# Optimization experiments

Measured on AMD Instinct MI355X. Metric: run time of the kernel, lower is better.

The kernel has to match this reference:

```python
import jax, jax.numpy as jnp
import numpy as np

K_WIN = 3  # fixed kernel width in the original module
PAD = (K_WIN - 1) // 2


def setup_inputs() -> dict:
    key = jax.random.key(0)
    k1, k2, k3 = jax.random.split(key, 3)
    B, L, D, T = 32, 2048, 256, 64
    x = jax.random.normal(k1, (B, L, D), dtype=jnp.float32)
    C = jax.random.normal(k2, (T, D), dtype=jnp.float32) * (1.0 / np.sqrt(D))
    W_den = jax.random.normal(k3, (D, K_WIN * D), dtype=jnp.float32) * (1.0 / np.sqrt(D))
    b_den = jnp.zeros((K_WIN * D,), dtype=jnp.float32)
    return {"x": x, "C": C, "W_den": W_den, "b_den": b_den}


def reference(x, C, W_den, b_den):
    B, L, D = x.shape
    T = C.shape[0]
    # kc = relu(C @ W + b): [T, k*D] -> [T, k, D]
    kc = jax.nn.relu(C @ W_den + b_den).reshape(T, K_WIN, D)
    # att = x @ C^T: [B, L, T]
    att = jnp.einsum('bld,td->blt', x, C)
    # per-position dynamic kernels: [B, L, k, D]
    ki = jnp.einsum('blt,tkd->blkd', att, kc)
    # sliding windows of padded x: [B, L, k, D]
    x_pad = jnp.pad(x, ((0, 0), (PAD, PAD), (0, 0)))
    windows = jnp.stack([x_pad[:, j:j + L, :] for j in range(K_WIN)], axis=2)
    # windowed multiply-sum over k: [B, L, D]
    return jnp.sum(windows * ki, axis=2)
```

## Files before the change

kernel.cpp:

```cpp
#include <hip/hip_runtime.h>

#define B_  32
#define L_  2048
#define D_  256
#define T_  64
#define KW  3
#define ROWS  16
#define XROWS 18

typedef float f32x4 __attribute__((ext_vector_type(4)));
typedef short s16x8 __attribute__((ext_vector_type(8)));
typedef short s16x4 __attribute__((ext_vector_type(4)));

__device__ __forceinline__ short f2bf(float f) {
    unsigned u = __builtin_bit_cast(unsigned, f);
    u += 0x7FFFu + ((u >> 16) & 1u);
    return (short)(u >> 16);
}
__device__ __forceinline__ float bf2f(short s) {
    unsigned u = ((unsigned)(unsigned short)s) << 16;
    return __builtin_bit_cast(float, u);
}

__global__ __launch_bounds__(256) void prep_kernel(const float* __restrict__ C,
                                                   const float* __restrict__ W,
                                                   const float* __restrict__ bias,
                                                   short* __restrict__ CbfPk,
                                                   short* __restrict__ kcPk) {
    __shared__ float Ws[256 * 16];
    const int tid = threadIdx.x;

    if (blockIdx.x < 16) {
        const int i0 = (blockIdx.x * 256 + tid) * 4;
        const int t = i0 >> 8, d = i0 & 255;
        const f32x4 v = *(const f32x4*)(C + i0);
        s16x4 s;
        s[0] = f2bf(v[0]); s[1] = f2bf(v[1]); s[2] = f2bf(v[2]); s[3] = f2bf(v[3]);
        const int tt = t >> 4, c = t & 15, ks = d >> 5, gg = (d >> 3) & 3, e = d & 7;
        *(s16x4*)&CbfPk[(((tt * 8 + ks) * 4 + gg) * 16 + c) * 8 + e] = s;
        return;
    }

    const int nb = blockIdx.x - 16;
    const int n0 = nb * 16;

    for (int idx = tid; idx < 256 * 16; idx += 256) {
        const int dd = idx >> 4, nl = idx & 15;
        Ws[idx] = W[dd * (KW * D_) + n0 + nl];
    }
    __syncthreads();

    const int t  = tid >> 2;
    const int nl = tid & 3;
    float acc[4];
    #pragma unroll
    for (int i = 0; i < 4; ++i) acc[i] = bias[n0 + nl + 4 * i];

    const float* Crow = C + t * D_;
    for (int dd = 0; dd < D_; ++dd) {
        const float cv = Crow[dd];
        #pragma unroll
        for (int i = 0; i < 4; ++i)
            acc[i] = fmaf(cv, Ws[dd * 16 + nl + 4 * i], acc[i]);
    }
    const int ks = t >> 5, gg = (t >> 3) & 3, e = t & 7;
    #pragma unroll
    for (int i = 0; i < 4; ++i) {
        const int cc = nl + 4 * i;
        kcPk[(((nb * 2 + ks) * 4 + gg) * 16 + cc) * 8 + e] = f2bf(fmaxf(acc[i], 0.f));
    }
}

#define XST 264
#define ATS 72

__global__ __launch_bounds__(256, 8) void main_kernel(const float* __restrict__ x,
                                                      const short* __restrict__ CbfPk,
                                                      const short* __restrict__ kcPk,
                                                      float* __restrict__ out) {
    __shared__ short xs[XROWS * XST];
    __shared__ short atts[ROWS * ATS];

    const int tid  = threadIdx.x;
    const int w    = tid >> 6;
    const int lane = tid & 63;
    const int c    = lane & 15;
    const int g    = lane >> 4;
    const int l0   = blockIdx.x * ROWS;
    const int b    = blockIdx.y;

    const f32x4* x4 = (const f32x4*)(x + (size_t)b * L_ * D_);
    for (int idx = tid; idx < XROWS * 64; idx += 256) {
        const int row = idx >> 6;
        const int d4  = idx & 63;
        const int l   = l0 - 1 + row;
        f32x4 v = {0.f, 0.f, 0.f, 0.f};
        if (l >= 0 && l < L_) v = x4[(size_t)l * 64 + d4];
        s16x4 s;
        s[0] = f2bf(v[0]); s[1] = f2bf(v[1]); s[2] = f2bf(v[2]); s[3] = f2bf(v[3]);
        *(s16x4*)&xs[row * XST + d4 * 4] = s;
    }
    __syncthreads();

    {
        f32x4 acc = (f32x4){0.f, 0.f, 0.f, 0.f};
        #pragma unroll
        for (int ks = 0; ks < 8; ++ks) {
            const s16x8 bf = *(const s16x8*)&CbfPk[(((w * 8 + ks) * 4 + g) * 16 + c) * 8];
            const s16x8 a  = *(const s16x8*)&xs[(1 + c) * XST + ks * 32 + g * 8];
            acc = __builtin_amdgcn_mfma_f32_16x16x32_bf16(a, bf, acc, 0, 0, 0);
        }
        #pragma unroll
        for (int r = 0; r < 4; ++r)
            atts[(g * 4 + r) * ATS + w * 16 + c] = f2bf(acc[r]);
    }
    __syncthreads();

    s16x8 afr[2];
    #pragma unroll
    for (int ks = 0; ks < 2; ++ks)
        afr[ks] = *(const s16x8*)&atts[c * ATS + ks * 32 + g * 8];

    const size_t outBase = ((size_t)b * L_ + l0) * D_;

    #pragma unroll
    for (int dtl = 0; dtl < 4; ++dtl) {
        const int dcol    = w * 64 + dtl * 16 + c;
        const int nb_base = w * 4 + dtl;
        s16x8 bfr[3][2];
        #pragma unroll
        for (int j = 0; j < 3; ++j)
            #pragma unroll
            for (int ks = 0; ks < 2; ++ks)
                bfr[j][ks] = *(const s16x8*)&kcPk[((((j * 16 + nb_base) * 2 + ks) * 4 + g) * 16 + c) * 8];

        f32x4 a0 = (f32x4){0.f,0.f,0.f,0.f};
        f32x4 a1 = (f32x4){0.f,0.f,0.f,0.f};
        f32x4 a2 = (f32x4){0.f,0.f,0.f,0.f};
        a0 = __builtin_amdgcn_mfma_f32_16x16x32_bf16(afr[0], bfr[0][0], a0, 0, 0, 0);
        a0 = __builtin_amdgcn_mfma_f32_16x16x32_bf16(afr[1], bfr[0][1], a0, 0, 0, 0);
        a1 = __builtin_amdgcn_mfma_f32_16x16x32_bf16(afr[0], bfr[1][0], a1, 0, 0, 0);
        a1 = __builtin_amdgcn_mfma_f32_16x16x32_bf16(afr[1], bfr[1][1], a1, 0, 0, 0);
        a2 = __builtin_amdgcn_mfma_f32_16x16x32_bf16(afr[0], bfr[2][0], a2, 0, 0, 0);
        a2 = __builtin_amdgcn_mfma_f32_16x16x32_bf16(afr[1], bfr[2][1], a2, 0, 0, 0);

        float xv[6];
        #pragma unroll
        for (int i = 0; i < 6; ++i)
            xv[i] = bf2f(xs[(g * 4 + i) * XST + dcol]);

        #pragma unroll
        for (int r = 0; r < 4; ++r) {
            const float o = a0[r] * xv[r] + a1[r] * xv[r + 1] + a2[r] * xv[r + 2];
            out[outBase + (size_t)(g * 4 + r) * D_ + dcol] = o;
        }
    }
}

extern "C" void kernel_launch(void* const* d_in, const int* in_sizes, int n_in,
                              void* d_out, int out_size, void* d_ws, size_t ws_size,
                              hipStream_t stream) {
    const float* x    = (const float*)d_in[0];
    const float* C    = (const float*)d_in[1];
    const float* Wden = (const float*)d_in[2];
    const float* bden = (const float*)d_in[3];
    float* out = (float*)d_out;

    short* kcPk  = (short*)d_ws;
    short* CbfPk = (short*)d_ws + KW * D_ * T_;

    prep_kernel<<<dim3(64), dim3(256), 0, stream>>>(C, Wden, bden, CbfPk, kcPk);

    dim3 grid(L_ / ROWS, B_);
    main_kernel<<<grid, dim3(256), 0, stream>>>(x, CbfPk, kcPk, out);
}
```

Baseline: 52.40 us.

## Process 32 rows per block with register-staged x loads and shared kc fragments

Each block now handles 32 sequence rows instead of 16. It issues all global x loads into registers up front, converts the first half to bf16 and runs the first attention MFMA pass while the second half's loads are still in flight. The kc B-fragments are loaded once and reused for both 16-row tiles, and halo rows are shared, which cuts redundant global traffic and per-block overhead. The cost is more registers and LDS per block, with occupancy lowered to 7 and half as many blocks.

```diff
diff --git a/kernel.cpp b/kernel.cpp
--- a/kernel.cpp
+++ b/kernel.cpp
@@ -5,8 +5,7 @@
 #define D_  256
 #define T_  64
 #define KW  3
-#define ROWS  16
-#define XROWS 18
+#define XROWS 34
 
 typedef float f32x4 __attribute__((ext_vector_type(4)));
 typedef short s16x8 __attribute__((ext_vector_type(8)));
@@ -74,86 +73,134 @@
 #define XST 264
 #define ATS 72
 
-__global__ __launch_bounds__(256, 8) void main_kernel(const float* __restrict__ x,
+__device__ __forceinline__ void phase1(const short* xs, short* atts_t,
+                                       const short* __restrict__ CbfPk,
+                                       int w, int g, int c, int ro) {
+    f32x4 acc = (f32x4){0.f, 0.f, 0.f, 0.f};
+    const short* xr = &xs[(ro + 1 + c) * XST];
+    #pragma unroll
+    for (int ks = 0; ks < 8; ++ks) {
+        const s16x8 cb = *(const s16x8*)&CbfPk[(((w * 8 + ks) * 4 + g) * 16 + c) * 8];
+        const s16x8 a  = *(const s16x8*)&xr[ks * 32 + g * 8];
+        acc = __builtin_amdgcn_mfma_f32_16x16x32_bf16(a, cb, acc, 0, 0, 0);
+    }
+    #pragma unroll
+    for (int r = 0; r < 4; ++r)
+        atts_t[(g * 4 + r) * ATS + w * 16 + c] = f2bf(acc[r]);
+}
+
+__device__ __forceinline__ void ph2_tile(s16x8 af0, s16x8 af1,
+                                         s16x8 b0, s16x8 b1, s16x8 b2,
+                                         s16x8 b3, s16x8 b4, s16x8 b5,
+                                         const short* xs, int ro,
+                                         float* __restrict__ out, size_t outBase,
+                                         int g, int c, int dcol) {
+    f32x4 a0 = (f32x4){0.f,0.f,0.f,0.f};
+    f32x4 a1 = (f32x4){0.f,0.f,0.f,0.f};
+    f32x4 a2 = (f32x4){0.f,0.f,0.f,0.f};
+    a0 = __builtin_amdgcn_mfma_f32_16x16x32_bf16(af0, b0, a0, 0, 0, 0);
+    a0 = __builtin_amdgcn_mfma_f32_16x16x32_bf16(af1, b1, a0, 0, 0, 0);
+    a1 = __builtin_amdgcn_mfma_f32_16x16x32_bf16(af0, b2, a1, 0, 0, 0);
+    a1 = __builtin_amdgcn_mfma_f32_16x16x32_bf16(af1, b3, a1, 0, 0, 0);
+    a2 = __builtin_amdgcn_mfma_f32_16x16x32_bf16(af0, b4, a2, 0, 0, 0);
+    a2 = __builtin_amdgcn_mfma_f32_16x16x32_bf16(af1, b5, a2, 0, 0, 0);
+
+    float xv[6];
+    #pragma unroll
+    for (int i = 0; i < 6; ++i)
+        xv[i] = bf2f(xs[(ro + g * 4 + i) * XST + dcol]);
+
+    #pragma unroll
+    for (int r = 0; r < 4; ++r) {
+        const float o = a0[r] * xv[r] + a1[r] * xv[r + 1] + a2[r] * xv[r + 2];
+        out[outBase + (size_t)(ro + g * 4 + r) * D_ + dcol] = o;
+    }
+}
+
+__global__ __launch_bounds__(256, 7) void main_kernel(const float* __restrict__ x,
                                                       const short* __restrict__ CbfPk,
                                                       const short* __restrict__ kcPk,
                                                       float* __restrict__ out) {
     __shared__ short xs[XROWS * XST];
-    __shared__ short atts[ROWS * ATS];
+    __shared__ short atts0[16 * ATS];
+    __shared__ short atts1[16 * ATS];
 
     const int tid  = threadIdx.x;
     const int w    = tid >> 6;
     const int lane = tid & 63;
     const int c    = lane & 15;
     const int g    = lane >> 4;
-    const int l0   = blockIdx.x * ROWS;
+    const int l0a  = blockIdx.x * 32;
     const int b    = blockIdx.y;
 
     const f32x4* x4 = (const f32x4*)(x + (size_t)b * L_ * D_);
-    for (int idx = tid; idx < XROWS * 64; idx += 256) {
-        const int row = idx >> 6;
-        const int d4  = idx & 63;
-        const int l   = l0 - 1 + row;
-        f32x4 v = {0.f, 0.f, 0.f, 0.f};
-        if (l >= 0 && l < L_) v = x4[(size_t)l * 64 + d4];
+
+    f32x4 rA[5];
+    #pragma unroll
+    for (int k = 0; k < 5; ++k) {
+        const int idx = tid + k * 256;
+        if (idx < 18 * 64) {
+            const int l = l0a - 1 + (idx >> 6);
+            rA[k] = (l >= 0 && l < L_) ? x4[(size_t)l * 64 + (idx & 63)]
+                                       : (f32x4){0.f, 0.f, 0.f, 0.f};
+        }
+    }
+    f32x4 rB[4];
+    #pragma unroll
+    for (int k = 0; k < 4; ++k) {
+        const int idx = tid + k * 256;
+        const int l = l0a + 17 + (idx >> 6);
+        rB[k] = (l < L_) ? x4[(size_t)l * 64 + (idx & 63)]
+                         : (f32x4){0.f, 0.f, 0.f, 0.f};
+    }
+
+    #pragma unroll
+    for (int k = 0; k < 5; ++k) {
+        const int idx = tid + k * 256;
+        if (idx < 18 * 64) {
+            s16x4 s;
+            s[0] = f2bf(rA[k][0]); s[1] = f2bf(rA[k][1]);
+            s[2] = f2bf(rA[k][2]); s[3] = f2bf(rA[k][3]);
+            *(s16x4*)&xs[(idx >> 6) * XST + (idx & 63) * 4] = s;
+        }
+    }
+    __syncthreads();
+
+    phase1(xs, atts0, CbfPk, w, g, c, 0);
+
+    #pragma unroll
+    for (int k = 0; k < 4; ++k) {
+        const int idx = tid + k * 256;
         s16x4 s;
-        s[0] = f2bf(v[0]); s[1] = f2bf(v[1]); s[2] = f2bf(v[2]); s[3] = f2bf(v[3]);
-        *(s16x4*)&xs[row * XST + d4 * 4] = s;
-    }
-    __syncthreads();
-
-    {
-        f32x4 acc = (f32x4){0.f, 0.f, 0.f, 0.f};
-        #pragma unroll
-        for (int ks = 0; ks < 8; ++ks) {
-            const s16x8 bf = *(const s16x8*)&CbfPk[(((w * 8 + ks) * 4 + g) * 16 + c) * 8];
-            const s16x8 a  = *(const s16x8*)&xs[(1 + c) * XST + ks * 32 + g * 8];
-            acc = __builtin_amdgcn_mfma_f32_16x16x32_bf16(a, bf, acc, 0, 0, 0);
-        }
-        #pragma unroll
-        for (int r = 0; r < 4; ++r)
-            atts[(g * 4 + r) * ATS + w * 16 + c] = f2bf(acc[r]);
-    }
-    __syncthreads();
-
-    s16x8 afr[2];
-    #pragma unroll
-    for (int ks = 0; ks < 2; ++ks)
-        afr[ks] = *(const s16x8*)&atts[c * ATS + ks * 32 + g * 8];
-
-    const size_t outBase = ((size_t)b * L_ + l0) * D_;
+        s[0] = f2bf(rB[k][0]); s[1] = f2bf(rB[k][1]);
+        s[2] = f2bf(rB[k][2]); s[3] = f2bf(rB[k][3]);
+        *(s16x4*)&xs[(18 + (idx >> 6)) * XST + (idx & 63) * 4] = s;
+    }
+    __syncthreads();
+
+    phase1(xs, atts1, CbfPk, w, g, c, 16);
+    __syncthreads();
+
+    const s16x8 af0a = *(const s16x8*)&atts0[c * ATS + 0 * 32 + g * 8];
+    const s16x8 af1a = *(const s16x8*)&atts0[c * ATS + 1 * 32 + g * 8];
+    const s16x8 af0b = *(const s16x8*)&atts1[c * ATS + 0 * 32 + g * 8];
+    const s16x8 af1b = *(const s16x8*)&atts1[c * ATS + 1 * 32 + g * 8];
+
+    const size_t outBase = ((size_t)b * L_ + l0a) * D_;
 
     #pragma unroll
     for (int dtl = 0; dtl < 4; ++dtl) {
-        const int dcol    = w * 64 + dtl * 16 + c;
-        const int nb_base = w * 4 + dtl;
-        s16x8 bfr[3][2];
-        #pragma unroll
-        for (int j = 0; j < 3; ++j)
-            #pragma unroll
-            for (int ks = 0; ks < 2; ++ks)
-                bfr[j][ks] = *(const s16x8*)&kcPk[((((j * 16 + nb_base) * 2 + ks) * 4 + g) * 16 + c) * 8];
-
-        f32x4 a0 = (f32x4){0.f,0.f,0.f,0.f};
-        f32x4 a1 = (f32x4){0.f,0.f,0.f,0.f};
-        f32x4 a2 = (f32x4){0.f,0.f,0.f,0.f};
-        a0 = __builtin_amdgcn_mfma_f32_16x16x32_bf16(afr[0], bfr[0][0], a0, 0, 0, 0);
-        a0 = __builtin_amdgcn_mfma_f32_16x16x32_bf16(afr[1], bfr[0][1], a0, 0, 0, 0);
-        a1 = __builtin_amdgcn_mfma_f32_16x16x32_bf16(afr[0], bfr[1][0], a1, 0, 0, 0);
-        a1 = __builtin_amdgcn_mfma_f32_16x16x32_bf16(afr[1], bfr[1][1], a1, 0, 0, 0);
-        a2 = __builtin_amdgcn_mfma_f32_16x16x32_bf16(afr[0], bfr[2][0], a2, 0, 0, 0);
-        a2 = __builtin_amdgcn_mfma_f32_16x16x32_bf16(afr[1], bfr[2][1], a2, 0, 0, 0);
-
-        float xv[6];
-        #pragma unroll
-        for (int i = 0; i < 6; ++i)
-            xv[i] = bf2f(xs[(g * 4 + i) * XST + dcol]);
-
-        #pragma unroll
-        for (int r = 0; r < 4; ++r) {
-            const float o = a0[r] * xv[r] + a1[r] * xv[r + 1] + a2[r] * xv[r + 2];
-            out[outBase + (size_t)(g * 4 + r) * D_ + dcol] = o;
-        }
+        const int dcol = w * 64 + dtl * 16 + c;
+        const int nbb  = w * 4 + dtl;
+        const s16x8 b0 = *(const s16x8*)&kcPk[((((0 * 16 + nbb) * 2 + 0) * 4 + g) * 16 + c) * 8];
+        const s16x8 b1 = *(const s16x8*)&kcPk[((((0 * 16 + nbb) * 2 + 1) * 4 + g) * 16 + c) * 8];
+        const s16x8 b2 = *(const s16x8*)&kcPk[((((1 * 16 + nbb) * 2 + 0) * 4 + g) * 16 + c) * 8];
+        const s16x8 b3 = *(const s16x8*)&kcPk[((((1 * 16 + nbb) * 2 + 1) * 4 + g) * 16 + c) * 8];
+        const s16x8 b4 = *(const s16x8*)&kcPk[((((2 * 16 + nbb) * 2 + 0) * 4 + g) * 16 + c) * 8];
+        const s16x8 b5 = *(const s16x8*)&kcPk[((((2 * 16 + nbb) * 2 + 1) * 4 + g) * 16 + c) * 8];
+
+        ph2_tile(af0a, af1a, b0, b1, b2, b3, b4, b5, xs, 0,  out, outBase, g, c, dcol);
+        ph2_tile(af0b, af1b, b0, b1, b2, b3, b4, b5, xs, 16, out, outBase, g, c, dcol);
     }
 }
 
@@ -171,6 +218,6 @@
 
     prep_kernel<<<dim3(64), dim3(256), 0, stream>>>(C, Wden, bden, CbfPk, kcPk);
 
-    dim3 grid(L_ / ROWS, B_);
+    dim3 grid(L_ / 32, B_);
     main_kernel<<<grid, dim3(256), 0, stream>>>(x, CbfPk, kcPk, out);
 }
```

Result: slower. 70.66 us (+34.9%).

## Process two batches per block to reuse C and kernel fragments

Applied to the files above, without the earlier changes.

Each block now handles the same 16-row tile for two batch indices. The C and kc B-fragments loaded from global memory are shared between both batches, and the grid is halved. This doubles LDS use and register pressure and lowers the occupancy hint from 8 to 6. The kernel is mostly bound by memory traffic for x and out, so the saved fragment loads may matter little.

```diff
diff --git a/kernel.cpp b/kernel.cpp
--- a/kernel.cpp
+++ b/kernel.cpp
@@ -74,12 +74,14 @@
 #define XST 264
 #define ATS 72
 
-__global__ __launch_bounds__(256, 8) void main_kernel(const float* __restrict__ x,
+__global__ __launch_bounds__(256, 6) void main_kernel(const float* __restrict__ x,
                                                       const short* __restrict__ CbfPk,
                                                       const short* __restrict__ kcPk,
                                                       float* __restrict__ out) {
-    __shared__ short xs[XROWS * XST];
-    __shared__ short atts[ROWS * ATS];
+    __shared__ short xs0[XROWS * XST];
+    __shared__ short xs1[XROWS * XST];
+    __shared__ short atts0[ROWS * ATS];
+    __shared__ short atts1[ROWS * ATS];
 
     const int tid  = threadIdx.x;
     const int w    = tid >> 6;
@@ -87,72 +89,103 @@
     const int c    = lane & 15;
     const int g    = lane >> 4;
     const int l0   = blockIdx.x * ROWS;
-    const int b    = blockIdx.y;
-
-    const f32x4* x4 = (const f32x4*)(x + (size_t)b * L_ * D_);
-    for (int idx = tid; idx < XROWS * 64; idx += 256) {
-        const int row = idx >> 6;
-        const int d4  = idx & 63;
+    const int b0   = blockIdx.y * 2;
+
+    const f32x4* x4a = (const f32x4*)(x + (size_t)b0 * L_ * D_);
+    const f32x4* x4b = (const f32x4*)(x + (size_t)(b0 + 1) * L_ * D_);
+    for (int idx = tid; idx < 2 * XROWS * 64; idx += 256) {
+        const int bb  = idx >= XROWS * 64;
+        const int rem = bb ? idx - XROWS * 64 : idx;
+        const int row = rem >> 6;
+        const int d4  = rem & 63;
         const int l   = l0 - 1 + row;
         f32x4 v = {0.f, 0.f, 0.f, 0.f};
-        if (l >= 0 && l < L_) v = x4[(size_t)l * 64 + d4];
+        if (l >= 0 && l < L_) v = (bb ? x4b : x4a)[(size_t)l * 64 + d4];
         s16x4 s;
         s[0] = f2bf(v[0]); s[1] = f2bf(v[1]); s[2] = f2bf(v[2]); s[3] = f2bf(v[3]);
-        *(s16x4*)&xs[row * XST + d4 * 4] = s;
+        *(s16x4*)&(bb ? xs1 : xs0)[row * XST + d4 * 4] = s;
     }
     __syncthreads();
 
     {
-        f32x4 acc = (f32x4){0.f, 0.f, 0.f, 0.f};
+        f32x4 acc0 = (f32x4){0.f, 0.f, 0.f, 0.f};
+        f32x4 acc1 = (f32x4){0.f, 0.f, 0.f, 0.f};
+        const short* xr0 = &xs0[(1 + c) * XST];
+        const short* xr1 = &xs1[(1 + c) * XST];
         #pragma unroll
         for (int ks = 0; ks < 8; ++ks) {
-            const s16x8 bf = *(const s16x8*)&CbfPk[(((w * 8 + ks) * 4 + g) * 16 + c) * 8];
-            const s16x8 a  = *(const s16x8*)&xs[(1 + c) * XST + ks * 32 + g * 8];
-            acc = __builtin_amdgcn_mfma_f32_16x16x32_bf16(a, bf, acc, 0, 0, 0);
+            const s16x8 cb = *(const s16x8*)&CbfPk[(((w * 8 + ks) * 4 + g) * 16 + c) * 8];
+            const s16x8 a0 = *(const s16x8*)&xr0[ks * 32 + g * 8];
+            const s16x8 a1 = *(const s16x8*)&xr1[ks * 32 + g * 8];
+            acc0 = __builtin_amdgcn_mfma_f32_16x16x32_bf16(a0, cb, acc0, 0, 0, 0);
+            acc1 = __builtin_amdgcn_mfma_f32_16x16x32_bf16(a1, cb, acc1, 0, 0, 0);
         }
         #pragma unroll
-        for (int r = 0; r < 4; ++r)
-            atts[(g * 4 + r) * ATS + w * 16 + c] = f2bf(acc[r]);
+        for (int r = 0; r < 4; ++r) {
+            atts0[(g * 4 + r) * ATS + w * 16 + c] = f2bf(acc0[r]);
+            atts1[(g * 4 + r) * ATS + w * 16 + c] = f2bf(acc1[r]);
+        }
     }
     __syncthreads();
 
-    s16x8 afr[2];
-    #pragma unroll
-    for (int ks = 0; ks < 2; ++ks)
-        afr[ks] = *(const s16x8*)&atts[c * ATS + ks * 32 + g * 8];
-
-    const size_t outBase = ((size_t)b * L_ + l0) * D_;
+    const s16x8 af00 = *(const s16x8*)&atts0[c * ATS + 0 * 32 + g * 8];
+    const s16x8 af01 = *(const s16x8*)&atts0[c * ATS + 1 * 32 + g * 8];
+    const s16x8 af10 = *(const s16x8*)&atts1[c * ATS + 0 * 32 + g * 8];
+    const s16x8 af11 = *(const s16x8*)&atts1[c * ATS + 1 * 32 + g * 8];
+
+    const size_t outBase0 = ((size_t)b0 * L_ + l0) * D_;
+    const size_t outBase1 = ((size_t)(b0 + 1) * L_ + l0) * D_;
 
     #pragma unroll
     for (int dtl = 0; dtl < 4; ++dtl) {
-        const int dcol    = w * 64 + dtl * 16 + c;
-        const int nb_base = w * 4 + dtl;
-        s16x8 bfr[3][2];
-        #pragma unroll
-        for (int j = 0; j < 3; ++j)
-            #pragma unroll
-            for (int ks = 0; ks < 2; ++ks)
-                bfr[j][ks] = *(const s16x8*)&kcPk[((((j * 16 + nb_base) * 2 + ks) * 4 + g) * 16 + c) * 8];
-
-        f32x4 a0 = (f32x4){0.f,0.f,0.f,0.f};
-        f32x4 a1 = (f32x4){0.f,0.f,0.f,0.f};
-        f32x4 a2 = (f32x4){0.f,0.f,0.f,0.f};
-        a0 = __builtin_amdgcn_mfma_f32_16x16x32_bf16(afr[0], bfr[0][0], a0, 0, 0, 0);
-        a0 = __builtin_amdgcn_mfma_f32_16x16x32_bf16(afr[1], bfr[0][1], a0, 0, 0, 0);
-        a1 = __builtin_amdgcn_mfma_f32_16x16x32_bf16(afr[0], bfr[1][0], a1, 0, 0, 0);
-        a1 = __builtin_amdgcn_mfma_f32_16x16x32_bf16(afr[1], bfr[1][1], a1, 0, 0, 0);
-        a2 = __builtin_amdgcn_mfma_f32_16x16x32_bf16(afr[0], bfr[2][0], a2, 0, 0, 0);
-        a2 = __builtin_amdgcn_mfma_f32_16x16x32_bf16(afr[1], bfr[2][1], a2, 0, 0, 0);
-
-        float xv[6];
-        #pragma unroll
-        for (int i = 0; i < 6; ++i)
-            xv[i] = bf2f(xs[(g * 4 + i) * XST + dcol]);
-
-        #pragma unroll
-        for (int r = 0; r < 4; ++r) {
-            const float o = a0[r] * xv[r] + a1[r] * xv[r + 1] + a2[r] * xv[r + 2];
-            out[outBase + (size_t)(g * 4 + r) * D_ + dcol] = o;
+        const int dcol = w * 64 + dtl * 16 + c;
+        const int nbb  = w * 4 + dtl;
+        const s16x8 kb0 = *(const s16x8*)&kcPk[((((0 * 16 + nbb) * 2 + 0) * 4 + g) * 16 + c) * 8];
+        const s16x8 kb1 = *(const s16x8*)&kcPk[((((0 * 16 + nbb) * 2 + 1) * 4 + g) * 16 + c) * 8];
+        const s16x8 kb2 = *(const s16x8*)&kcPk[((((1 * 16 + nbb) * 2 + 0) * 4 + g) * 16 + c) * 8];
+        const s16x8 kb3 = *(const s16x8*)&kcPk[((((1 * 16 + nbb) * 2 + 1) * 4 + g) * 16 + c) * 8];
+        const s16x8 kb4 = *(const s16x8*)&kcPk[((((2 * 16 + nbb) * 2 + 0) * 4 + g) * 16 + c) * 8];
+        const s16x8 kb5 = *(const s16x8*)&kcPk[((((2 * 16 + nbb) * 2 + 1) * 4 + g) * 16 + c) * 8];
+
+        {
+            f32x4 a0 = (f32x4){0.f,0.f,0.f,0.f};
+            f32x4 a1 = (f32x4){0.f,0.f,0.f,0.f};
+            f32x4 a2 = (f32x4){0.f,0.f,0.f,0.f};
+            a0 = __builtin_amdgcn_mfma_f32_16x16x32_bf16(af00, kb0, a0, 0, 0, 0);
+            a0 = __builtin_amdgcn_mfma_f32_16x16x32_bf16(af01, kb1, a0, 0, 0, 0);
+            a1 = __builtin_amdgcn_mfma_f32_16x16x32_bf16(af00, kb2, a1, 0, 0, 0);
+            a1 = __builtin_amdgcn_mfma_f32_16x16x32_bf16(af01, kb3, a1, 0, 0, 0);
+            a2 = __builtin_amdgcn_mfma_f32_16x16x32_bf16(af00, kb4, a2, 0, 0, 0);
+            a2 = __builtin_amdgcn_mfma_f32_16x16x32_bf16(af01, kb5, a2, 0, 0, 0);
+            float xv[6];
+            #pragma unroll
+            for (int i = 0; i < 6; ++i)
+                xv[i] = bf2f(xs0[(g * 4 + i) * XST + dcol]);
+            #pragma unroll
+            for (int r = 0; r < 4; ++r) {
+                const float o = a0[r] * xv[r] + a1[r] * xv[r + 1] + a2[r] * xv[r + 2];
+                out[outBase0 + (size_t)(g * 4 + r) * D_ + dcol] = o;
+            }
+        }
+        {
+            f32x4 a0 = (f32x4){0.f,0.f,0.f,0.f};
+            f32x4 a1 = (f32x4){0.f,0.f,0.f,0.f};
+            f32x4 a2 = (f32x4){0.f,0.f,0.f,0.f};
+            a0 = __builtin_amdgcn_mfma_f32_16x16x32_bf16(af10, kb0, a0, 0, 0, 0);
+            a0 = __builtin_amdgcn_mfma_f32_16x16x32_bf16(af11, kb1, a0, 0, 0, 0);
+            a1 = __builtin_amdgcn_mfma_f32_16x16x32_bf16(af10, kb2, a1, 0, 0, 0);
+            a1 = __builtin_amdgcn_mfma_f32_16x16x32_bf16(af11, kb3, a1, 0, 0, 0);
+            a2 = __builtin_amdgcn_mfma_f32_16x16x32_bf16(af10, kb4, a2, 0, 0, 0);
+            a2 = __builtin_amdgcn_mfma_f32_16x16x32_bf16(af11, kb5, a2, 0, 0, 0);
+            float xv[6];
+            #pragma unroll
+            for (int i = 0; i < 6; ++i)
+                xv[i] = bf2f(xs1[(g * 4 + i) * XST + dcol]);
+            #pragma unroll
+            for (int r = 0; r < 4; ++r) {
+                const float o = a0[r] * xv[r] + a1[r] * xv[r + 1] + a2[r] * xv[r + 2];
+                out[outBase1 + (size_t)(g * 4 + r) * D_ + dcol] = o;
+            }
         }
     }
 }
@@ -171,6 +204,6 @@
 
     prep_kernel<<<dim3(64), dim3(256), 0, stream>>>(C, Wden, bden, CbfPk, kcPk);
 
-    dim3 grid(L_ / ROWS, B_);
+    dim3 grid(L_ / ROWS, B_ / 2);
     main_kernel<<<grid, dim3(256), 0, stream>>>(x, CbfPk, kcPk, out);
 }
```

After: 59.65 us. +13.8%, slower.
